# Kernel optimization log

Measured on AMD Instinct MI355X. Metric: run time of the kernel, lower is better.

## Reference

```python
import jax, jax.numpy as jnp
import numpy as np

B, T, C, H = 4, 2048, 1024, 16
HD = C // H


def setup_inputs() -> dict:
    key = jax.random.key(0)
    ks = jax.random.split(key, 9)
    s = 1.0 / np.sqrt(C)
    return {
        "x": jax.random.normal(ks[0], (B, T, C), dtype=jnp.float32),
        "Wk": jax.random.uniform(ks[1], (C, C), jnp.float32, -s, s),
        "bk": jax.random.uniform(ks[2], (C,), jnp.float32, -s, s),
        "Wq": jax.random.uniform(ks[3], (C, C), jnp.float32, -s, s),
        "bq": jax.random.uniform(ks[4], (C,), jnp.float32, -s, s),
        "Wv": jax.random.uniform(ks[5], (C, C), jnp.float32, -s, s),
        "bv": jax.random.uniform(ks[6], (C,), jnp.float32, -s, s),
        "Wp": jax.random.uniform(ks[7], (C, C), jnp.float32, -s, s),
        "bp": jax.random.uniform(ks[8], (C,), jnp.float32, -s, s),
        "padding_mask": jnp.ones((B, T), dtype=jnp.int32),
    }


def reference(x, Wk, bk, Wq, bq, Wv, bv, Wp, bp, padding_mask):
    # torch nn.Linear: y = x @ W.T + b  (W is [out, in])
    def split_heads(t):  # [B,T,C] -> [B,H,T,HD]
        return t.reshape(B, T, H, HD).transpose(0, 2, 1, 3)

    k = split_heads(x @ Wk.T + bk)
    q = split_heads(x @ Wq.T + bq)
    v = split_heads(x @ Wv.T + bv)

    scale = 1.0 / jnp.sqrt(jnp.float32(HD))
    att = jnp.einsum("bhqd,bhkd->bhqk", q, k) * scale  # [B,H,T,T]

    causal = jnp.tril(jnp.ones((T, T), dtype=bool))  # [T,T]
    pad = (padding_mask != 0)[:, None, None, :]       # [B,1,1,T]
    mask = causal[None, None, :, :] & pad
    att = jnp.where(mask, att, -jnp.inf)
    att = jax.nn.softmax(att, axis=-1)

    y = jnp.einsum("bhqk,bhkd->bhqd", att, v)  # [B,H,T,HD]
    y = y.transpose(0, 2, 1, 3).reshape(B, T, C)
    return y @ Wp.T + bp
```

## Files before the change

### kernel.cpp

```cpp
#include <hip/hip_runtime.h>
#include <hip/hip_bf16.h>
#include <math.h>
#include <stdint.h>

#define BB 4
#define TT 2048
#define CC 1024
#define HH 16
#define HD 64
#define MM (BB*TT)
#define NQT 8
#define SCQ 0.180336878f

using f32x4  = __attribute__((ext_vector_type(4))) float;
using f32x16 = __attribute__((ext_vector_type(16))) float;
using i32x4  = __attribute__((ext_vector_type(4))) int;
using bf16x4 = __attribute__((ext_vector_type(4))) __bf16;
using bf16x8 = __attribute__((ext_vector_type(8))) __bf16;

__device__ __forceinline__ float fast_exp2(float x) {
  return __builtin_amdgcn_exp2f(x);
}

__device__ __forceinline__ int cvt_pk_bf16(float lo, float hi_) {
  int r;
  asm("v_cvt_pk_bf16_f32 %0, %1, %2" : "=v"(r) : "v"(lo), "v"(hi_));
  return r;
}

__device__ __forceinline__ void gload_lds16(const void* g, void* l) {
  __builtin_amdgcn_global_load_lds(
      (__attribute__((address_space(1))) void*)(void*)(g),
      (__attribute__((address_space(3))) void*)(l), 16, 0, 0);
}

__global__ __launch_bounds__(256)
void cvt_f32_bf16(const float* __restrict__ s, __bf16* __restrict__ d, int n4) {
  int i = blockIdx.x * 256 + threadIdx.x;
  if (i >= n4) return;
  float4 v = ((const float4*)s)[i];
  bf16x4 o;
  o[0] = (__bf16)v.x; o[1] = (__bf16)v.y; o[2] = (__bf16)v.z; o[3] = (__bf16)v.w;
  *(bf16x4*)(d + (size_t)i * 4) = o;
}

__global__ __launch_bounds__(256)
void cvt_w4(const float* __restrict__ Wq, const float* __restrict__ Wk,
            const float* __restrict__ Wv, const float* __restrict__ Wp,
            __bf16* __restrict__ wqkv, __bf16* __restrict__ wpb) {
  int which = blockIdx.y;
  const float* s = which == 0 ? Wq : which == 1 ? Wk : which == 2 ? Wv : Wp;
  __bf16* d = which == 3 ? wpb : wqkv + (size_t)which * CC * CC;
  float sc = which == 0 ? SCQ : 1.f;
  int i = blockIdx.x * 256 + threadIdx.x;
  float4 v = ((const float4*)s)[i];
  bf16x4 o;
  o[0] = (__bf16)(v.x * sc); o[1] = (__bf16)(v.y * sc);
  o[2] = (__bf16)(v.z * sc); o[3] = (__bf16)(v.w * sc);
  *(bf16x4*)(d + (size_t)i * 4) = o;
}

#define WAITV6 asm volatile("s_waitcnt vmcnt(6)" ::: "memory")
#define WAITV4 asm volatile("s_waitcnt vmcnt(4)" ::: "memory")
#define WAITV2 asm volatile("s_waitcnt vmcnt(2)" ::: "memory")
#define WAITV0 asm volatile("s_waitcnt vmcnt(0)" ::: "memory")
#define WAITL0 asm volatile("s_waitcnt lgkmcnt(0)" ::: "memory")
#define BARR   __builtin_amdgcn_s_barrier()
#define SB0    __builtin_amdgcn_sched_barrier(0)
#define PRIO1  __builtin_amdgcn_s_setprio(1)
#define PRIO0  __builtin_amdgcn_s_setprio(0)

#define LDA_SET(buf, mq)                                                      \
  {                                                                           \
    const char* base_ = (const char*)&LA[buf][mq][0] + (wm * 64 + lq) * 128;  \
    _Pragma("unroll")                                                         \
    for (int m4 = 0; m4 < 4; ++m4)                                            \
      _Pragma("unroll")                                                       \
      for (int kk = 0; kk < 2; ++kk)                                          \
        a[m4 * 2 + kk] =                                                      \
            *(const bf16x8*)(base_ + m4 * 2048 + ((kk * 64 + g * 16) ^ swz)); \
  }

#define LDB_SET(buf, nq)                                                      \
  {                                                                           \
    const char* base_ = (const char*)&LB[buf][nq][0] + (wn * 32 + lq) * 128;  \
    _Pragma("unroll")                                                         \
    for (int n2 = 0; n2 < 2; ++n2)                                            \
      _Pragma("unroll")                                                       \
      for (int kk = 0; kk < 2; ++kk)                                          \
        b[nq][n2 * 2 + kk] =                                                  \
            *(const bf16x8*)(base_ + n2 * 2048 + ((kk * 64 + g * 16) ^ swz)); \
  }

#define STAGE_A(nbuf, h, tt)                                                  \
  {                                                                           \
    const char* s_ = Ag + ((size_t)((h)*128 + srow)) * 2048 + (tt)*128 + scol1; \
    gload_lds16(s_, (char*)&LA[nbuf][h][0] + so16);                           \
    gload_lds16(s_ + (size_t)64 * 2048, (char*)&LA[nbuf][h][0] + so16 + 8192);\
  }

#define STAGE_B(nbuf, h, tt)                                                  \
  {                                                                           \
    const char* s_ = Bg + ((size_t)((h)*128 + srow)) * 2048 + (tt)*128 + scol1; \
    gload_lds16(s_, (char*)&LB[nbuf][h][0] + so16);                           \
    gload_lds16(s_ + (size_t)64 * 2048, (char*)&LB[nbuf][h][0] + so16 + 8192);\
  }

#define MFMA_PH(mq, nq)                                                       \
  _Pragma("unroll")                                                           \
  for (int m4 = 0; m4 < 4; ++m4)                                              \
    _Pragma("unroll")                                                         \
    for (int n2 = 0; n2 < 2; ++n2)                                            \
      _Pragma("unroll")                                                       \
      for (int kk = 0; kk < 2; ++kk)                                          \
        acc[mq][m4][nq][n2] = __builtin_amdgcn_mfma_f32_16x16x32_bf16(        \
            a[m4 * 2 + kk], b[nq][n2 * 2 + kk], acc[mq][m4][nq][n2], 0, 0, 0);

__global__ __launch_bounds__(512, 2)
void gemm_qkv(const __bf16* __restrict__ A, const __bf16* __restrict__ Bm,
              const float* __restrict__ b0, const float* __restrict__ b1,
              const float* __restrict__ b2, __bf16* __restrict__ out,
              __bf16* __restrict__ vt) {
  __shared__ __bf16 LA[2][2][128 * 64];
  __shared__ __bf16 LB[2][2][128 * 64];
  const int tid = threadIdx.x, wid = tid >> 6, lane = tid & 63;
  const int g = lane >> 4, lq = lane & 15;
  const int wm = wid >> 2, wn = wid & 3;
  const int bm = blockIdx.x / 12, bn = blockIdx.x % 12;
  const int brow = bm << 8, bcol = bn << 8;
  const int swz = (lq & 7) << 4;

  const int srow = tid >> 3, so16 = tid * 16;
  const int scol1 = ((tid & 7) << 4) ^ ((srow & 7) << 4);
  const char* Ag = (const char*)A + (size_t)brow * 2048;
  const char* Bg = (const char*)Bm + (size_t)bcol * 2048;

  f32x4 acc[2][4][2][2] = {};
  bf16x8 a[8], b[2][4];

  STAGE_A(0, 0, 0); STAGE_B(0, 0, 0); STAGE_B(0, 1, 0); STAGE_A(0, 1, 0);
  STAGE_A(1, 0, 1); STAGE_B(1, 0, 1); STAGE_B(1, 1, 1);
  WAITV6; BARR;

#pragma unroll 1
  for (int t = 0; t < 8; ++t) {
    const bool s2 = (t < 7);
    const int k1 = 2 * t + 1, k2 = 2 * t + 2, k3 = 2 * t + 3;
    LDA_SET(0, 0); LDB_SET(0, 0);
    STAGE_A(1, 1, k1);
    BARR; WAITL0; SB0;
    PRIO1; MFMA_PH(0, 0); PRIO0; BARR;
    LDB_SET(0, 1);
    if (s2) STAGE_A(0, 0, k2);
    BARR; WAITL0; SB0;
    PRIO1; MFMA_PH(0, 1); PRIO0; BARR;
    LDA_SET(0, 1);
    if (s2) STAGE_B(0, 0, k2);
    BARR; WAITL0; SB0;
    PRIO1; MFMA_PH(1, 1); PRIO0; BARR;
    if (s2) { STAGE_B(0, 1, k2); WAITV6; } else { WAITV0; }
    BARR; SB0;
    PRIO1; MFMA_PH(1, 0); PRIO0; BARR;
    LDA_SET(1, 0); LDB_SET(1, 0);
    if (s2) STAGE_A(0, 1, k2);
    BARR; WAITL0; SB0;
    PRIO1; MFMA_PH(0, 0); PRIO0; BARR;
    LDB_SET(1, 1);
    if (s2) STAGE_A(1, 0, k3);
    BARR; WAITL0; SB0;
    PRIO1; MFMA_PH(0, 1); PRIO0; BARR;
    LDA_SET(1, 1);
    if (s2) STAGE_B(1, 0, k3);
    BARR; WAITL0; SB0;
    PRIO1; MFMA_PH(1, 1); PRIO0; BARR;
    if (s2) { STAGE_B(1, 1, k3); WAITV6; }
    BARR; SB0;
    PRIO1; MFMA_PH(1, 0); PRIO0; BARR;
  }

  const int proj = bn >> 2;
  if (proj < 2) {
    const float* bias = proj == 0 ? b0 : b1;
    const float bsc = proj == 0 ? SCQ : 1.f;
#pragma unroll
    for (int mq = 0; mq < 2; ++mq)
#pragma unroll
      for (int nq = 0; nq < 2; ++nq)
#pragma unroll
        for (int n2 = 0; n2 < 2; ++n2) {
          int col = bcol + nq * 128 + wn * 32 + n2 * 16 + lq;
          int cw = col & (CC - 1);
          float bb = bias[cw] * bsc;
          int h_ = cw >> 6, d_ = cw & (HD - 1);
#pragma unroll
          for (int m4 = 0; m4 < 4; ++m4) {
            int row0 = brow + mq * 128 + wm * 64 + m4 * 16 + g * 4;
#pragma unroll
            for (int i = 0; i < 4; ++i) {
              int row = row0 + i;
              int b_ = row >> 11, t_ = row & (TT - 1);
              out[((size_t)proj << 23) +
                  ((((size_t)b_ * HH + h_) * TT + t_) << 6) + d_] =
                  (__bf16)(acc[mq][m4][nq][n2][i] + bb);
            }
          }
        }
  } else {
    __bf16* lt = (__bf16*)&LA[0][0][0];
    const int cv0 = (bn & 3) << 8;
    const int b_ = brow >> 11, t0 = brow & (TT - 1);
    const int hbase = (bn & 3) << 2;
    const int rd_d = tid >> 3, rd_tb = (tid & 7) << 5;
#pragma unroll
    for (int cc = 0; cc < 4; ++cc) {
      if ((wn >> 1) == (cc & 1)) {
#pragma unroll
        for (int n2 = 0; n2 < 2; ++n2) {
          int c = ((wn & 1) << 5) + (n2 << 4) + lq;
          float bb = b2[cv0 + (cc << 6) + c];
#pragma unroll
          for (int mq = 0; mq < 2; ++mq)
#pragma unroll
            for (int m4 = 0; m4 < 4; ++m4) {
              int r = (mq << 7) + (wm << 6) + (m4 << 4) + (g << 2);
              bf16x4 pk;
#pragma unroll
              for (int i = 0; i < 4; ++i)
                pk[i] = (__bf16)(acc[mq][m4][cc >> 1][n2][i] + bb);
              *(bf16x4*)(lt + c * 264 + r) = pk;
            }
        }
      }
      __syncthreads();
      __bf16* dst = vt + (((size_t)((b_ * HH + hbase + cc) * HD + rd_d)) << 11)
                       + t0 + rd_tb;
      const __bf16* srcl = lt + rd_d * 264 + rd_tb;
#pragma unroll
      for (int j = 0; j < 4; ++j)
        *(bf16x8*)(dst + j * 8) = *(const bf16x8*)(srcl + j * 8);
      __syncthreads();
    }
  }
}

__global__ __launch_bounds__(256, 2)
void gemm_proj(const __bf16* __restrict__ A, const __bf16* __restrict__ Bm,
               const float* __restrict__ bias, float* __restrict__ out,
               int M, int N, int K) {
  __shared__ __bf16 As[128 * 32];
  __shared__ __bf16 Bs[128 * 32];
  const int tid = threadIdx.x;
  const int wid = tid >> 6, lane = tid & 63;
  const int g = lane >> 4, lq = lane & 15;
  const int nbn = N >> 7;
  const int brow = (blockIdx.x / nbn) << 7;
  const int bcol = (blockIdx.x % nbn) << 7;
  const int wr = (wid >> 1) << 6, wc = (wid & 1) << 6;

  f32x4 acc[4][4] = {};

  const int o0 = wid * 2048 + lane * 16;
  for (int kt = 0; kt < K; kt += 32) {
    __syncthreads();
#pragma unroll
    for (int j = 0; j < 2; ++j) {
      int o = o0 + j * 1024;
      int row = o >> 6, colb = o & 63;
      gload_lds16((const char*)A + ((size_t)(brow + row) * K + kt) * 2 + colb,
                  (char*)As + o);
      gload_lds16((const char*)Bm + ((size_t)(bcol + row) * K + kt) * 2 + colb,
                  (char*)Bs + o);
    }
    __syncthreads();
    bf16x8 av[4], bv[4];
#pragma unroll
    for (int m = 0; m < 4; ++m)
      av[m] = *(const bf16x8*)(As + (wr + m * 16 + lq) * 32 + g * 8);
#pragma unroll
    for (int n = 0; n < 4; ++n)
      bv[n] = *(const bf16x8*)(Bs + (wc + n * 16 + lq) * 32 + g * 8);
#pragma unroll
    for (int m = 0; m < 4; ++m)
#pragma unroll
      for (int n = 0; n < 4; ++n)
        acc[m][n] = __builtin_amdgcn_mfma_f32_16x16x32_bf16(av[m], bv[n], acc[m][n], 0, 0, 0);
  }

#pragma unroll
  for (int m = 0; m < 4; ++m) {
#pragma unroll
    for (int n = 0; n < 4; ++n) {
      int col = bcol + wc + n * 16 + lq;
      float bb = bias[col];
      int row0 = brow + wr + m * 16 + g * 4;
#pragma unroll
      for (int i = 0; i < 4; ++i)
        out[(size_t)(row0 + i) * N + col] = acc[m][n][i] + bb;
    }
  }
}

__global__ __launch_bounds__(512, 3)
void attn_fwd(const __bf16* __restrict__ Q, const __bf16* __restrict__ K,
              const __bf16* __restrict__ Vt, const int* __restrict__ pm,
              __bf16* __restrict__ Y) {
  __shared__ __bf16 Ks[3][64 * 64];
  __shared__ __bf16 Vs[3][64 * 64];
  __shared__ int flg;
  const int tid = threadIdx.x, wid = tid >> 6, lane = tid & 63;
  const int l31 = lane & 31, hi = lane >> 5;
  const int bx = blockIdx.x;
  const int bh = bx & 63, jj = bx >> 6;
  const int r2 = ((jj & 1) << 1) | ((jj >> 1) & 1);
  const int qi = (jj & 4) ? r2 : 7 - r2;
  const int b_ = bh >> 4, h_ = bh & 15;
  const __bf16* Qb = Q + (size_t)bh * TT * HD;
  const __bf16* Kb = K + (size_t)bh * TT * HD;
  const __bf16* Vb = Vt + (size_t)bh * HD * TT;
  const int* pmb = pm + b_ * TT;

  const int so = tid * 16;
  const int srow = so >> 7, scol = (so & 127) ^ ((srow & 7) << 4);

  const int q0 = qi << 8;
  const int qw = q0 + wid * 32;
  const int ntiles = 4 * qi + 4;
  const int sw0 = (l31 & 7) << 4;

  bf16x8 qf[4];
#pragma unroll
  for (int s = 0; s < 4; ++s)
    qf[s] = *(const bf16x8*)(Qb + (size_t)(qw + l31) * HD + s * 16 + hi * 8);

  int4 pm4 = ((const int4*)pmb)[tid];
  bool okp = pm4.x && pm4.y && pm4.z && pm4.w;
  if (tid == 0) flg = 1;

  const char* ksrc = (const char*)Kb + (size_t)srow * 128 + scol;
  const char* vsrc = (const char*)Vb + (size_t)srow * (TT * 2) + scol;
  char* kdst = (char*)&Ks[0][0] + so;
  char* vdst = (char*)&Vs[0][0] + so;

#pragma unroll
  for (int n = 0; n < 3; ++n) {
    gload_lds16(ksrc + (size_t)n * 8192, kdst + n * 8192);
    gload_lds16(vsrc + (size_t)n * 128, vdst + n * 8192);
  }
  WAITL0; BARR; SB0;
  if (!okp) flg = 0;
  WAITL0; WAITV4; BARR; SB0;
  const bool allones = (flg != 0);

  f32x16 o0 = {}, o1 = {};
  float lsum = 0.f;
  float m = -INFINITY;

  int cur = 0;
#pragma unroll 1
  for (int t = 0; t < ntiles; ++t) {
    const int kv0 = t << 6;
    unsigned long long bits = ~0ull;
    if (__builtin_expect(!allones, 0)) {
      int pmv = pmb[kv0 + lane];
      bits = __ballot(pmv != 0);
    }

    if (kv0 <= qw + 31) {
      const char* VsC = (const char*)&Vs[0][0] + cur * 8192;

#pragma unroll
      for (int h = 0; h < 2; ++h) {
        const int kvh = kv0 + 32 * h;
        if (kvh <= qw + 31) {
          const char* KsC =
              (const char*)&Ks[0][0] + cur * 8192 + (32 * h + l31) * 128;
          f32x16 S = {};
          __builtin_amdgcn_s_setprio(1);
#pragma unroll
          for (int s = 0; s < 4; ++s) {
            bf16x8 kf = *(const bf16x8*)(KsC + ((32 * s + 16 * hi) ^ sw0));
            S = __builtin_amdgcn_mfma_f32_32x32x16_bf16(kf, qf[s], S, 0, 0, 0);
          }
          __builtin_amdgcn_s_setprio(0);

          if (__builtin_expect(bits != ~0ull, 0)) {
#pragma unroll
            for (int r = 0; r < 16; ++r) {
              const int c = (r & 3) + 8 * (r >> 2);
              if (!((bits >> (32 * h + c + 4 * hi)) & 1ull)) S[r] = -INFINITY;
            }
          }
          if (kvh + 31 > qw) {
            const int thr = qw + l31 - kvh - 4 * hi;
#pragma unroll
            for (int r = 0; r < 16; ++r) {
              const int c = (r & 3) + 8 * (r >> 2);
              S[r] = (c <= thr) ? S[r] : -INFINITY;
            }
          }

          float t0 = fmaxf(fmaxf(S[0], S[1]), fmaxf(S[2], S[3]));
          float t1 = fmaxf(fmaxf(S[4], S[5]), fmaxf(S[6], S[7]));
          float t2 = fmaxf(fmaxf(S[8], S[9]), fmaxf(S[10], S[11]));
          float t3 = fmaxf(fmaxf(S[12], S[13]), fmaxf(S[14], S[15]));
          float pmax = fmaxf(fmaxf(t0, t1), fmaxf(t2, t3));
          if (!__all(pmax <= m + 8.f)) {
            float nm = fmaxf(pmax, __shfl_xor(pmax, 32));
            float mn = fmaxf(m, nm);
            float c = fast_exp2(m - mn);
            m = mn;
            lsum *= c;
#pragma unroll
            for (int r = 0; r < 16; ++r) {
              float cr = __shfl(c, (r & 3) + 8 * (r >> 2) + 4 * hi);
              o0[r] *= cr;
              o1[r] *= cr;
            }
          }

#pragma unroll
          for (int r = 0; r < 16; ++r) S[r] = fast_exp2(S[r] - m);
          {
            float u0 = (S[0] + S[1]) + (S[2] + S[3]);
            float u1 = (S[4] + S[5]) + (S[6] + S[7]);
            float u2 = (S[8] + S[9]) + (S[10] + S[11]);
            float u3 = (S[12] + S[13]) + (S[14] + S[15]);
            lsum += (u0 + u1) + (u2 + u3);
          }

          __builtin_amdgcn_s_setprio(1);
#pragma unroll
          for (int s = 0; s < 2; ++s) {
            const int ub = 2 * s;
            int A0 = cvt_pk_bf16(S[4 * ub + 0], S[4 * ub + 1]);
            int A1 = cvt_pk_bf16(S[4 * ub + 2], S[4 * ub + 3]);
            int B0 = cvt_pk_bf16(S[4 * ub + 4], S[4 * ub + 5]);
            int B1 = cvt_pk_bf16(S[4 * ub + 6], S[4 * ub + 7]);
            int s0 = hi ? A0 : B0, s1 = hi ? A1 : B1;
            int e0 = __shfl_xor(s0, 32), e1 = __shfl_xor(s1, 32);
            i32x4 wv;
            wv[0] = hi ? e0 : A0;
            wv[1] = hi ? e1 : A1;
            wv[2] = hi ? B0 : e0;
            wv[3] = hi ? B1 : e1;
            bf16x8 pa = __builtin_bit_cast(bf16x8, wv);
            const int co = 64 * h + 32 * s + 16 * hi;
            bf16x8 v0 = *(const bf16x8*)(VsC + l31 * 128 + (co ^ sw0));
            bf16x8 v1 = *(const bf16x8*)(VsC + (32 + l31) * 128 + (co ^ sw0));
            o0 = __builtin_amdgcn_mfma_f32_32x32x16_bf16(pa, v0, o0, 0, 0, 0);
            o1 = __builtin_amdgcn_mfma_f32_32x32x16_bf16(pa, v1, o1, 0, 0, 0);
          }
          __builtin_amdgcn_s_setprio(0);
          __builtin_amdgcn_sched_barrier(0);
        }
      }
    }

    BARR; SB0;
    if (t + 3 < ntiles) {
      gload_lds16(ksrc + (size_t)(t + 3) * 8192, kdst + cur * 8192);
      gload_lds16(vsrc + (size_t)(t + 3) * 128, vdst + cur * 8192);
      WAITV4;
    } else if (t + 2 < ntiles) {
      WAITV2;
    } else if (t + 1 < ntiles) {
      WAITV0;
    }
    BARR; SB0;
    cur = (cur == 2) ? 0 : cur + 1;
  }

  float linv = 1.f / (lsum + __shfl_xor(lsum, 32));
#pragma unroll
  for (int r = 0; r < 16; ++r) {
    const int crow = (r & 3) + 8 * (r >> 2) + 4 * hi;
    float ir = __shfl(linv, crow);
    const int qrow = qw + crow;
    __bf16* yp = Y + ((size_t)(b_ * TT + qrow)) * CC + h_ * HD + l31;
    yp[0]  = (__bf16)(o0[r] * ir);
    yp[32] = (__bf16)(o1[r] * ir);
  }
}

extern "C" void kernel_launch(void* const* d_in, const int* in_sizes, int n_in,
                              void* d_out, int out_size, void* d_ws, size_t ws_size,
                              hipStream_t stream) {
  (void)in_sizes; (void)n_in; (void)out_size; (void)ws_size;
  const float* x  = (const float*)d_in[0];
  const float* Wk = (const float*)d_in[1];
  const float* bk = (const float*)d_in[2];
  const float* Wq = (const float*)d_in[3];
  const float* bq = (const float*)d_in[4];
  const float* Wv = (const float*)d_in[5];
  const float* bv = (const float*)d_in[6];
  const float* Wp = (const float*)d_in[7];
  const float* bp = (const float*)d_in[8];
  const int* pmask = (const int*)d_in[9];

  char* ws = (char*)d_ws;
  const size_t MB = 1024 * 1024;
  __bf16* xb   = (__bf16*)(ws);
  __bf16* wqkv = (__bf16*)(ws + 16 * MB);
  __bf16* wpb  = (__bf16*)(ws + 22 * MB);
  __bf16* qb   = (__bf16*)(ws + 24 * MB);
  __bf16* kb   = qb + ((size_t)1 << 23);
  __bf16* vtb  = (__bf16*)(ws + 56 * MB);
  __bf16* yb   = xb;

  int n4 = (MM * CC) / 4;
  cvt_f32_bf16<<<(n4 + 255) / 256, 256, 0, stream>>>(x, xb, n4);
  cvt_w4<<<dim3((CC * CC / 4) / 256, 4), 256, 0, stream>>>(
      Wq, Wk, Wv, Wp, wqkv, wpb);

  gemm_qkv<<<(MM / 256) * (3 * CC / 256), 512, 0, stream>>>(
      xb, wqkv, bq, bk, bv, qb, vtb);

  attn_fwd<<<NQT * BB * HH, 512, 0, stream>>>(qb, kb, vtb, pmask, yb);

  gemm_proj<<<(MM / 128) * (CC / 128), 256, 0, stream>>>(
      yb, wpb, bp, (float*)d_out, MM, CC, CC);
}
```

Measured before the change: 195.7 us.

## Split attention into 128-row query tiles with 256-thread blocks and reworked prefetch

The attention kernel now uses 256-thread blocks covering 128 query rows each and launches twice as many blocks, with a new query-tile ordering meant to balance causal work. The K/V triple-buffer pipeline is restructured so the wait and barrier come at the top of each iteration and the prefetch runs two tiles ahead with one barrier per tile instead of two. The max, exp-subtract and sum reductions are rewritten with packed two-wide float vectors, and the first QK MFMA starts from a zero accumulator. This aims for finer load balance, more resident waves and lower sync overhead, at the cost of more redundant Q and mask loads across blocks.

```diff
diff --git a/kernel.cpp b/kernel.cpp
--- a/kernel.cpp
+++ b/kernel.cpp
@@ -9,9 +9,10 @@
 #define HH 16
 #define HD 64
 #define MM (BB*TT)
-#define NQT 8
+#define NQT2 16
 #define SCQ 0.180336878f
 
+using f32x2  = __attribute__((ext_vector_type(2))) float;
 using f32x4  = __attribute__((ext_vector_type(4))) float;
 using f32x16 = __attribute__((ext_vector_type(16))) float;
 using i32x4  = __attribute__((ext_vector_type(4))) int;
@@ -26,6 +27,10 @@
   int r;
   asm("v_cvt_pk_bf16_f32 %0, %1, %2" : "=v"(r) : "v"(lo), "v"(hi_));
   return r;
+}
+
+__device__ __forceinline__ f32x2 max2(f32x2 a, f32x2 b) {
+  return __builtin_elementwise_max(a, b);
 }
 
 __device__ __forceinline__ void gload_lds16(const void* g, void* l) {
@@ -62,7 +67,6 @@
 
 #define WAITV6 asm volatile("s_waitcnt vmcnt(6)" ::: "memory")
 #define WAITV4 asm volatile("s_waitcnt vmcnt(4)" ::: "memory")
-#define WAITV2 asm volatile("s_waitcnt vmcnt(2)" ::: "memory")
 #define WAITV0 asm volatile("s_waitcnt vmcnt(0)" ::: "memory")
 #define WAITL0 asm volatile("s_waitcnt lgkmcnt(0)" ::: "memory")
 #define BARR   __builtin_amdgcn_s_barrier()
@@ -300,7 +304,7 @@
   }
 }
 
-__global__ __launch_bounds__(512, 3)
+__global__ __launch_bounds__(256, 3)
 void attn_fwd(const __bf16* __restrict__ Q, const __bf16* __restrict__ K,
               const __bf16* __restrict__ Vt, const int* __restrict__ pm,
               __bf16* __restrict__ Y) {
@@ -311,8 +315,7 @@
   const int l31 = lane & 31, hi = lane >> 5;
   const int bx = blockIdx.x;
   const int bh = bx & 63, jj = bx >> 6;
-  const int r2 = ((jj & 1) << 1) | ((jj >> 1) & 1);
-  const int qi = (jj & 4) ? r2 : 7 - r2;
+  const int qi = 4 * (jj >> 2) + ((jj + (jj >> 2)) & 3);
   const int b_ = bh >> 4, h_ = bh & 15;
   const __bf16* Qb = Q + (size_t)bh * TT * HD;
   const __bf16* Kb = K + (size_t)bh * TT * HD;
@@ -320,38 +323,46 @@
   const int* pmb = pm + b_ * TT;
 
   const int so = tid * 16;
-  const int srow = so >> 7, scol = (so & 127) ^ ((srow & 7) << 4);
-
-  const int q0 = qi << 8;
+  const int srow = tid >> 3;
+  const int scol = (so & 127) ^ ((srow & 7) << 4);
+
+  const int q0 = qi << 7;
   const int qw = q0 + wid * 32;
-  const int ntiles = 4 * qi + 4;
+  const int ntiles = 2 * qi + 2;
   const int sw0 = (l31 & 7) << 4;
 
   bf16x8 qf[4];
 #pragma unroll
   for (int s = 0; s < 4; ++s)
     qf[s] = *(const bf16x8*)(Qb + (size_t)(qw + l31) * HD + s * 16 + hi * 8);
-
-  int4 pm4 = ((const int4*)pmb)[tid];
-  bool okp = pm4.x && pm4.y && pm4.z && pm4.w;
+  SB0;
+
+  int4 pa4 = ((const int4*)pmb)[tid];
+  int4 pb4 = ((const int4*)pmb)[tid + 256];
+  bool okp = pa4.x && pa4.y && pa4.z && pa4.w &&
+             pb4.x && pb4.y && pb4.z && pb4.w;
   if (tid == 0) flg = 1;
-
-  const char* ksrc = (const char*)Kb + (size_t)srow * 128 + scol;
-  const char* vsrc = (const char*)Vb + (size_t)srow * (TT * 2) + scol;
-  char* kdst = (char*)&Ks[0][0] + so;
-  char* vdst = (char*)&Vs[0][0] + so;
-
-#pragma unroll
-  for (int n = 0; n < 3; ++n) {
-    gload_lds16(ksrc + (size_t)n * 8192, kdst + n * 8192);
-    gload_lds16(vsrc + (size_t)n * 128, vdst + n * 8192);
-  }
-  WAITL0; BARR; SB0;
+  __syncthreads();
   if (!okp) flg = 0;
-  WAITL0; WAITV4; BARR; SB0;
+
+#pragma unroll
+  for (int n = 0; n < 2; ++n) {
+    char* kd = (char*)&Ks[0][0] + n * 8192 + so;
+    char* vd = (char*)&Vs[0][0] + n * 8192 + so;
+#pragma unroll
+    for (int j = 0; j < 2; ++j) {
+      gload_lds16((const char*)Kb + (size_t)(n * 64 + srow + 32 * j) * 128 + scol,
+                  kd + j * 4096);
+      gload_lds16((const char*)Vb + (size_t)(srow + 32 * j) * (TT * 2) +
+                      n * 128 + scol,
+                  vd + j * 4096);
+    }
+  }
+  __syncthreads();
   const bool allones = (flg != 0);
 
   f32x16 o0 = {}, o1 = {};
+  f32x16 vzero = {};
   float lsum = 0.f;
   float m = -INFINITY;
 
@@ -359,11 +370,26 @@
 #pragma unroll 1
   for (int t = 0; t < ntiles; ++t) {
     const int kv0 = t << 6;
+    if (t + 1 < ntiles) { WAITV4; } else { WAITV0; }
+    BARR; SB0;
+    if (t + 2 < ntiles) {
+      int stb = cur + 2; if (stb >= 3) stb -= 3;
+      char* kd = (char*)&Ks[0][0] + stb * 8192 + so;
+      char* vd = (char*)&Vs[0][0] + stb * 8192 + so;
+      const size_t nk = (size_t)(kv0 + 128);
+#pragma unroll
+      for (int j = 0; j < 2; ++j) {
+        gload_lds16((const char*)Kb + (nk + srow + 32 * j) * 128 + scol,
+                    kd + j * 4096);
+        gload_lds16((const char*)Vb + (size_t)(srow + 32 * j) * (TT * 2) +
+                        nk * 2 + scol,
+                    vd + j * 4096);
+      }
+    }
+
     unsigned long long bits = ~0ull;
-    if (__builtin_expect(!allones, 0)) {
-      int pmv = pmb[kv0 + lane];
-      bits = __ballot(pmv != 0);
-    }
+    if (__builtin_expect(!allones, 0))
+      bits = __ballot(pmb[kv0 + lane] != 0);
 
     if (kv0 <= qw + 31) {
       const char* VsC = (const char*)&Vs[0][0] + cur * 8192;
@@ -374,10 +400,14 @@
         if (kvh <= qw + 31) {
           const char* KsC =
               (const char*)&Ks[0][0] + cur * 8192 + (32 * h + l31) * 128;
-          f32x16 S = {};
+          f32x16 S;
           __builtin_amdgcn_s_setprio(1);
-#pragma unroll
-          for (int s = 0; s < 4; ++s) {
+          {
+            bf16x8 k0 = *(const bf16x8*)(KsC + ((16 * hi) ^ sw0));
+            S = __builtin_amdgcn_mfma_f32_32x32x16_bf16(k0, qf[0], vzero, 0, 0, 0);
+          }
+#pragma unroll
+          for (int s = 1; s < 4; ++s) {
             bf16x8 kf = *(const bf16x8*)(KsC + ((32 * s + 16 * hi) ^ sw0));
             S = __builtin_amdgcn_mfma_f32_32x32x16_bf16(kf, qf[s], S, 0, 0, 0);
           }
@@ -399,11 +429,15 @@
             }
           }
 
-          float t0 = fmaxf(fmaxf(S[0], S[1]), fmaxf(S[2], S[3]));
-          float t1 = fmaxf(fmaxf(S[4], S[5]), fmaxf(S[6], S[7]));
-          float t2 = fmaxf(fmaxf(S[8], S[9]), fmaxf(S[10], S[11]));
-          float t3 = fmaxf(fmaxf(S[12], S[13]), fmaxf(S[14], S[15]));
-          float pmax = fmaxf(fmaxf(t0, t1), fmaxf(t2, t3));
+          f32x2 x0 = {S[0], S[1]},  x1 = {S[2], S[3]};
+          f32x2 x2 = {S[4], S[5]},  x3 = {S[6], S[7]};
+          f32x2 x4 = {S[8], S[9]},  x5 = {S[10], S[11]};
+          f32x2 x6 = {S[12], S[13]}, x7 = {S[14], S[15]};
+          x0 = max2(x0, x4); x1 = max2(x1, x5);
+          x2 = max2(x2, x6); x3 = max2(x3, x7);
+          x0 = max2(x0, x2); x1 = max2(x1, x3);
+          x0 = max2(x0, x1);
+          float pmax = fmaxf(x0[0], x0[1]);
           if (!__all(pmax <= m + 8.f)) {
             float nm = fmaxf(pmax, __shfl_xor(pmax, 32));
             float mn = fmaxf(m, nm);
@@ -418,24 +452,32 @@
             }
           }
 
-#pragma unroll
-          for (int r = 0; r < 16; ++r) S[r] = fast_exp2(S[r] - m);
+          const f32x2 mm = {m, m};
+#pragma unroll
+          for (int r = 0; r < 16; r += 2) {
+            f32x2 u = {S[r], S[r + 1]};
+            u -= mm;
+            S[r] = fast_exp2(u[0]);
+            S[r + 1] = fast_exp2(u[1]);
+          }
           {
-            float u0 = (S[0] + S[1]) + (S[2] + S[3]);
-            float u1 = (S[4] + S[5]) + (S[6] + S[7]);
-            float u2 = (S[8] + S[9]) + (S[10] + S[11]);
-            float u3 = (S[12] + S[13]) + (S[14] + S[15]);
-            lsum += (u0 + u1) + (u2 + u3);
+            f32x2 u0 = {S[0], S[1]},  u1 = {S[2], S[3]};
+            f32x2 u2 = {S[4], S[5]},  u3 = {S[6], S[7]};
+            f32x2 u4 = {S[8], S[9]},  u5 = {S[10], S[11]};
+            f32x2 u6 = {S[12], S[13]}, u7 = {S[14], S[15]};
+            u0 += u4; u1 += u5; u2 += u6; u3 += u7;
+            u0 += u2; u1 += u3;
+            u0 += u1;
+            lsum += u0[0] + u0[1];
           }
 
           __builtin_amdgcn_s_setprio(1);
 #pragma unroll
           for (int s = 0; s < 2; ++s) {
-            const int ub = 2 * s;
-            int A0 = cvt_pk_bf16(S[4 * ub + 0], S[4 * ub + 1]);
-            int A1 = cvt_pk_bf16(S[4 * ub + 2], S[4 * ub + 3]);
-            int B0 = cvt_pk_bf16(S[4 * ub + 4], S[4 * ub + 5]);
-            int B1 = cvt_pk_bf16(S[4 * ub + 6], S[4 * ub + 7]);
+            int A0 = cvt_pk_bf16(S[8 * s + 0], S[8 * s + 1]);
+            int A1 = cvt_pk_bf16(S[8 * s + 2], S[8 * s + 3]);
+            int B0 = cvt_pk_bf16(S[8 * s + 4], S[8 * s + 5]);
+            int B1 = cvt_pk_bf16(S[8 * s + 6], S[8 * s + 7]);
             int s0 = hi ? A0 : B0, s1 = hi ? A1 : B1;
             int e0 = __shfl_xor(s0, 32), e1 = __shfl_xor(s1, 32);
             i32x4 wv;
@@ -451,22 +493,10 @@
             o1 = __builtin_amdgcn_mfma_f32_32x32x16_bf16(pa, v1, o1, 0, 0, 0);
           }
           __builtin_amdgcn_s_setprio(0);
-          __builtin_amdgcn_sched_barrier(0);
         }
       }
     }
-
-    BARR; SB0;
-    if (t + 3 < ntiles) {
-      gload_lds16(ksrc + (size_t)(t + 3) * 8192, kdst + cur * 8192);
-      gload_lds16(vsrc + (size_t)(t + 3) * 128, vdst + cur * 8192);
-      WAITV4;
-    } else if (t + 2 < ntiles) {
-      WAITV2;
-    } else if (t + 1 < ntiles) {
-      WAITV0;
-    }
-    BARR; SB0;
+    SB0;
     cur = (cur == 2) ? 0 : cur + 1;
   }
 
@@ -515,7 +545,7 @@
   gemm_qkv<<<(MM / 256) * (3 * CC / 256), 512, 0, stream>>>(
       xb, wqkv, bq, bk, bv, qb, vtb);
 
-  attn_fwd<<<NQT * BB * HH, 512, 0, stream>>>(qb, kb, vtb, pmask, yb);
+  attn_fwd<<<NQT2 * BB * HH, 256, 0, stream>>>(qb, kb, vtb, pmask, yb);
 
   gemm_proj<<<(MM / 128) * (CC / 128), 256, 0, stream>>>(
       yb, wpb, bp, (float*)d_out, MM, CC, CC);
```

New measurement: 183.1 us. -6.5%, faster.
